# Kernel tuning notes

Hardware: AMD Instinct MI355X
Metric: run time of the kernel (lower is better)

The kernel has to match this reference:

```python
import jax, jax.numpy as jnp
import numpy as np

N_NODES = 100000
N_EDGES = 1600000
F_IN, F_HID, F_OUT = 64, 64, 32


def setup_inputs() -> dict:
    key = jax.random.key(0)
    k1, k2, k3, k4 = jax.random.split(key, 4)
    x = jax.random.normal(k1, (N_NODES, F_IN), dtype=jnp.float32)
    edge_idx = jax.random.randint(k2, (2, N_EDGES), 0, N_NODES, dtype=jnp.int64)
    W1 = jax.random.normal(k3, (F_IN, F_HID), dtype=jnp.float32) * (1.0 / np.sqrt(F_IN))
    b1 = jnp.zeros((F_HID,), dtype=jnp.float32)
    W2 = jax.random.normal(k4, (F_HID, F_OUT), dtype=jnp.float32) * (1.0 / np.sqrt(F_HID))
    b2 = jnp.zeros((F_OUT,), dtype=jnp.float32)
    return {"x": x, "edge_idx": edge_idx, "W1": W1, "b1": b1, "W2": W2, "b2": b2}


def _gcn_conv(h, src, dst, norm, W, b, n):
    # PyG GCNConv: transform first, then normalized sum aggregation, then bias.
    h = h @ W                                   # [N, F_out]
    msg = h[src] * norm[:, None]                # [E+N, F_out] gather + scale
    agg = jax.ops.segment_sum(msg, dst, num_segments=n)  # scatter-add
    return agg + b


def reference(x, edge_idx, W1, b1, W2, b2):
    n = x.shape[0]
    loop = jnp.arange(n, dtype=edge_idx.dtype)
    src = jnp.concatenate([edge_idx[0], loop])  # add self-loops
    dst = jnp.concatenate([edge_idx[1], loop])
    # symmetric normalization D^-1/2 (A+I) D^-1/2
    deg = jax.ops.segment_sum(jnp.ones_like(dst, dtype=x.dtype), dst, num_segments=n)
    dinv = jnp.where(deg > 0, jax.lax.rsqrt(deg), 0.0)
    norm = dinv[src] * dinv[dst]                # [E+N]

    h = _gcn_conv(x, src, dst, norm, W1, b1, n)
    h = jax.nn.relu(h)
    # dropout(p=0.5) is identity in eval mode (deterministic reference)
    out = _gcn_conv(h, src, dst, norm, W2, b2, n)
    return out
```

## Files before the change

### kernel.cpp

```cpp
#include <hip/hip_runtime.h>
#include <hip/hip_bf16.h>
#include <hip/hip_fp16.h>


#define N_FEAT_IN 64
#define B2SHIFT 9
#define CHUNK 4096
#define PADSTRIDE 3592

struct alignas(8) half4 { __half2 lo, hi; };
struct alignas(16) half8 { __half2 h[4]; };

__global__ __launch_bounds__(1024) void passA_hist(const int* __restrict__ dst,
                                                   int* __restrict__ H, int E) {
    __shared__ int h[256];
    int t = threadIdx.x;
    if (t < 256) h[t] = 0;
    __syncthreads();
    int base = blockIdx.x * CHUNK;
    int end = min(base + CHUNK, E);
    for (int i = base + t; i < end; i += 1024)
        atomicAdd(&h[dst[i] >> B2SHIFT], 1);
    __syncthreads();
    if (t < 256) H[blockIdx.x * 256 + t] = h[t];
}

__global__ __launch_bounds__(512) void col_scan_a(int* __restrict__ H,
                                                  int* __restrict__ ctot, int NR) {
    __shared__ int s[512];
    int b = blockIdx.x;
    int t = threadIdx.x;
    int v = (t < NR) ? H[t * 256 + b] : 0;
    s[t] = v;
    __syncthreads();
    for (int off = 1; off < 512; off <<= 1) {
        int a = (t >= off) ? s[t - off] : 0;
        __syncthreads();
        s[t] += a;
        __syncthreads();
    }
    if (t < NR) H[t * 256 + b] = s[t] - v;
    if (t == 511) ctot[b] = s[511];
}

__global__ __launch_bounds__(256) void col_scan_b(const int* __restrict__ ctot,
                                                  int* __restrict__ cbase,
                                                  int* __restrict__ bbase,
                                                  int* __restrict__ row_ptr,
                                                  int NB, int n, int E) {
    __shared__ int s[256];
    int t = threadIdx.x;
    int v = ctot[t];
    s[t] = v;
    __syncthreads();
    for (int off = 1; off < 256; off <<= 1) {
        int a = (t >= off) ? s[t - off] : 0;
        __syncthreads();
        s[t] += a;
        __syncthreads();
    }
    int e = s[t] - v;
    cbase[t] = e;
    if (t < NB) bbase[t] = e;
    if (t == 0) { bbase[NB] = E; row_ptr[n] = E; }
}

__global__ __launch_bounds__(1024) void passB_place(const int* __restrict__ src,
                                                    const int* __restrict__ dst,
                                                    const int* __restrict__ H,
                                                    const int* __restrict__ cbase,
                                                    unsigned* __restrict__ bedges, int E) {
    __shared__ int cur[256];
    int t = threadIdx.x;
    if (t < 256) cur[t] = H[blockIdx.x * 256 + t] + cbase[t];
    __syncthreads();
    int base = blockIdx.x * CHUNK;
    int end = min(base + CHUNK, E);
    for (int i = base + t; i < end; i += 1024) {
        int d = dst[i];
        int p = atomicAdd(&cur[d >> B2SHIFT], 1);
        bedges[p] = ((unsigned)src[i] << B2SHIFT) | (unsigned)(d & 511);
    }
}

__global__ __launch_bounds__(1024) void bucket_csr(const int* __restrict__ bbase,
                                                   const unsigned* __restrict__ bedges,
                                                   int* __restrict__ row_ptr,
                                                   int* __restrict__ rend,
                                                   float* __restrict__ dinv,
                                                   int* __restrict__ csr_src, int n) {
    __shared__ int lh[512];
    __shared__ int cur[512];
    int t = threadIdx.x;
    if (t < 512) lh[t] = 0;
    __syncthreads();
    int b = blockIdx.x;
    int beg = bbase[b], end = bbase[b + 1];
    for (int i = beg + t; i < end; i += 1024)
        atomicAdd(&lh[bedges[i] & 511], 1);
    __syncthreads();
    int c = (t < 512) ? lh[t] : 0;
    __syncthreads();
    int cp = (c + 7) & ~7;
    if (t < 512) lh[t] = cp;
    __syncthreads();
    for (int off = 1; off < 512; off <<= 1) {
        int a = (t < 512 && t >= off) ? lh[t - off] : 0;
        __syncthreads();
        if (t < 512) lh[t] += a;
        __syncthreads();
    }
    int pb = ((beg + 7) & ~7) + b * PADSTRIDE;
    if (t < 512) {
        int d = (b << B2SHIFT) + t;
        int rbeg = pb + lh[t] - cp;
        cur[t] = rbeg;
        if (d < n) {
            row_ptr[d] = rbeg;
            rend[d] = rbeg + cp;
            dinv[d] = rsqrtf((float)c + 1.0f);
            for (int i = c; i < cp; ++i) csr_src[rbeg + i] = n;
        }
    }
    __syncthreads();
    for (int i = beg + t; i < end; i += 1024) {
        unsigned v = bedges[i];
        int p = atomicAdd(&cur[v & 511], 1);
        csr_src[p] = (int)(v >> B2SHIFT);
    }
}

__global__ __launch_bounds__(256) void gemm64(const float* __restrict__ A,
                                              const float* __restrict__ W,
                                              const float* __restrict__ dinv,
                                              __half* __restrict__ outh, int n) {
    constexpr int K = 64, FO = 64, CPT = 16;
    __shared__ float As[64][K + 4];
    __shared__ float Ws[K][FO];

    const int t = threadIdx.x;
    const int r0 = blockIdx.x * 64;

    if (blockIdx.x == 0 && t < FO)
        outh[(size_t)n * FO + t] = __float2half(0.f);

    for (int i = t; i < K * FO / 4; i += 256) {
        int k = i / (FO / 4);
        int c4 = (i % (FO / 4)) * 4;
        *(float4*)&Ws[k][c4] = *(const float4*)&W[k * FO + c4];
    }
    for (int i = t; i < 1024; i += 256) {
        int row = i / 16;
        int c4 = (i % 16) * 4;
        int g = r0 + row;
        float4 v = make_float4(0.f, 0.f, 0.f, 0.f);
        if (g < n) v = *(const float4*)&A[(size_t)g * K + c4];
        *(float4*)&As[row][c4] = v;
    }
    __syncthreads();

    const int row = t >> 2;
    const int c0 = (t & 3) * CPT;
    float acc[CPT];
#pragma unroll
    for (int j = 0; j < CPT; ++j) acc[j] = 0.f;
#pragma unroll
    for (int k = 0; k < K; ++k) {
        float xv = As[row][k];
#pragma unroll
        for (int j = 0; j < CPT; ++j) acc[j] = fmaf(xv, Ws[k][c0 + j], acc[j]);
    }

    int g = r0 + row;
    if (g < n) {
        float sc = dinv[g];
#pragma unroll
        for (int j4 = 0; j4 < CPT; j4 += 4) {
            half4 h;
            h.lo = __floats2half2_rn(acc[j4] * sc, acc[j4 + 1] * sc);
            h.hi = __floats2half2_rn(acc[j4 + 2] * sc, acc[j4 + 3] * sc);
            *(half4*)&outh[(size_t)g * FO + c0 + j4] = h;
        }
    }
}

#define ACC8(v)                                                       \
    {                                                                 \
        float2 f0 = __half22float2((v).h[0]);                         \
        float2 f1 = __half22float2((v).h[1]);                         \
        float2 f2 = __half22float2((v).h[2]);                         \
        float2 f3 = __half22float2((v).h[3]);                         \
        a0 += f0.x; a1 += f0.y; a2 += f1.x; a3 += f1.y;               \
        a4 += f2.x; a5 += f2.y; a6 += f3.x; a7 += f3.y;               \
    }

__global__ __launch_bounds__(256) void agg64(const int* __restrict__ row_ptr,
                                             const int* __restrict__ rend,
                                             const int* __restrict__ csr_src,
                                             const float* __restrict__ dinv,
                                             const __half* __restrict__ xs1,
                                             const float* __restrict__ b1,
                                             __half* __restrict__ th, int n) {
    int d = blockIdx.x * 32 + (threadIdx.x >> 3);
    if (d >= n) return;
    int c = threadIdx.x & 7;
    const half8* __restrict__ xrow = (const half8*)xs1 + c;

    half8 sv = xrow[(size_t)d * 8];
    float a0, a1, a2, a3, a4, a5, a6, a7;
    {
        float2 f0 = __half22float2(sv.h[0]), f1 = __half22float2(sv.h[1]);
        float2 f2 = __half22float2(sv.h[2]), f3 = __half22float2(sv.h[3]);
        a0 = f0.x; a1 = f0.y; a2 = f1.x; a3 = f1.y;
        a4 = f2.x; a5 = f2.y; a6 = f3.x; a7 = f3.y;
    }

    int beg = row_ptr[d];
    int end = rend[d];
    if (beg < end) {
        int4 ia = *(const int4*)&csr_src[beg];
        int4 ib = *(const int4*)&csr_src[beg + 4];
        int jb = beg;
        for (;;) {
            int jn = jb + 8;
            bool more = jn < end;
            int js = more ? jn : beg;
            int4 na = *(const int4*)&csr_src[js];
            int4 nb = *(const int4*)&csr_src[js + 4];
            half8 v0 = xrow[(size_t)ia.x * 8];
            half8 v1 = xrow[(size_t)ia.y * 8];
            half8 v2 = xrow[(size_t)ia.z * 8];
            half8 v3 = xrow[(size_t)ia.w * 8];
            half8 v4 = xrow[(size_t)ib.x * 8];
            half8 v5 = xrow[(size_t)ib.y * 8];
            half8 v6 = xrow[(size_t)ib.z * 8];
            half8 v7 = xrow[(size_t)ib.w * 8];
            ACC8(v0); ACC8(v1); ACC8(v2); ACC8(v3);
            ACC8(v4); ACC8(v5); ACC8(v6); ACC8(v7);
            if (!more) break;
            jb = jn; ia = na; ib = nb;
        }
    }

    float di = dinv[d];
    float4 ba = *(const float4*)&b1[8 * c];
    float4 bb = *(const float4*)&b1[8 * c + 4];
    float t0 = fmaxf(fmaf(di, a0, ba.x), 0.f);
    float t1 = fmaxf(fmaf(di, a1, ba.y), 0.f);
    float t2 = fmaxf(fmaf(di, a2, ba.z), 0.f);
    float t3 = fmaxf(fmaf(di, a3, ba.w), 0.f);
    float t4 = fmaxf(fmaf(di, a4, bb.x), 0.f);
    float t5 = fmaxf(fmaf(di, a5, bb.y), 0.f);
    float t6 = fmaxf(fmaf(di, a6, bb.z), 0.f);
    float t7 = fmaxf(fmaf(di, a7, bb.w), 0.f);
    half8 o;
    o.h[0] = __floats2half2_rn(t0, t1);
    o.h[1] = __floats2half2_rn(t2, t3);
    o.h[2] = __floats2half2_rn(t4, t5);
    o.h[3] = __floats2half2_rn(t6, t7);
    *(half8*)&th[(size_t)d * 64 + 8 * c] = o;
}

__global__ __launch_bounds__(256) void gemm32h(const __half* __restrict__ Ah,
                                               const float* __restrict__ W,
                                               const float* __restrict__ dinv,
                                               __half* __restrict__ outh, int n) {
    constexpr int K = 64, FO = 32, CPT = 8;
    __shared__ float As[64][K + 4];
    __shared__ float Ws[K][FO];

    const int t = threadIdx.x;
    const int r0 = blockIdx.x * 64;

    if (blockIdx.x == 0 && t < FO)
        outh[(size_t)n * FO + t] = __float2half(0.f);

    for (int i = t; i < K * FO / 4; i += 256) {
        int k = i / (FO / 4);
        int c4 = (i % (FO / 4)) * 4;
        *(float4*)&Ws[k][c4] = *(const float4*)&W[k * FO + c4];
    }
    for (int i = t; i < 1024; i += 256) {
        int row = i / 16;
        int c4 = (i % 16) * 4;
        int g = r0 + row;
        float4 v = make_float4(0.f, 0.f, 0.f, 0.f);
        if (g < n) {
            half4 hv = *(const half4*)&Ah[(size_t)g * K + c4];
            float2 lo = __half22float2(hv.lo), hi = __half22float2(hv.hi);
            v = make_float4(lo.x, lo.y, hi.x, hi.y);
        }
        *(float4*)&As[row][c4] = v;
    }
    __syncthreads();

    const int row = t >> 2;
    const int c0 = (t & 3) * CPT;
    float acc[CPT];
#pragma unroll
    for (int j = 0; j < CPT; ++j) acc[j] = 0.f;
#pragma unroll
    for (int k = 0; k < K; ++k) {
        float xv = As[row][k];
#pragma unroll
        for (int j = 0; j < CPT; ++j) acc[j] = fmaf(xv, Ws[k][c0 + j], acc[j]);
    }

    int g = r0 + row;
    if (g < n) {
        float sc = dinv[g];
#pragma unroll
        for (int j4 = 0; j4 < CPT; j4 += 4) {
            half4 h;
            h.lo = __floats2half2_rn(acc[j4] * sc, acc[j4 + 1] * sc);
            h.hi = __floats2half2_rn(acc[j4 + 2] * sc, acc[j4 + 3] * sc);
            *(half4*)&outh[(size_t)g * FO + c0 + j4] = h;
        }
    }
}

__global__ __launch_bounds__(256) void agg32(const int* __restrict__ row_ptr,
                                             const int* __restrict__ rend,
                                             const int* __restrict__ csr_src,
                                             const float* __restrict__ dinv,
                                             const __half* __restrict__ xs2,
                                             const float* __restrict__ b2,
                                             float* __restrict__ out, int n) {
    int d = blockIdx.x * 64 + (threadIdx.x >> 2);
    if (d >= n) return;
    int c = threadIdx.x & 3;
    const half8* __restrict__ xrow = (const half8*)xs2 + c;

    half8 sv = xrow[(size_t)d * 4];
    float a0, a1, a2, a3, a4, a5, a6, a7;
    {
        float2 f0 = __half22float2(sv.h[0]), f1 = __half22float2(sv.h[1]);
        float2 f2 = __half22float2(sv.h[2]), f3 = __half22float2(sv.h[3]);
        a0 = f0.x; a1 = f0.y; a2 = f1.x; a3 = f1.y;
        a4 = f2.x; a5 = f2.y; a6 = f3.x; a7 = f3.y;
    }

    int beg = row_ptr[d];
    int end = rend[d];
    if (beg < end) {
        int4 ia = *(const int4*)&csr_src[beg];
        int4 ib = *(const int4*)&csr_src[beg + 4];
        int jb = beg;
        for (;;) {
            int jn = jb + 8;
            bool more = jn < end;
            int js = more ? jn : beg;
            int4 na = *(const int4*)&csr_src[js];
            int4 nb = *(const int4*)&csr_src[js + 4];
            half8 v0 = xrow[(size_t)ia.x * 4];
            half8 v1 = xrow[(size_t)ia.y * 4];
            half8 v2 = xrow[(size_t)ia.z * 4];
            half8 v3 = xrow[(size_t)ia.w * 4];
            half8 v4 = xrow[(size_t)ib.x * 4];
            half8 v5 = xrow[(size_t)ib.y * 4];
            half8 v6 = xrow[(size_t)ib.z * 4];
            half8 v7 = xrow[(size_t)ib.w * 4];
            ACC8(v0); ACC8(v1); ACC8(v2); ACC8(v3);
            ACC8(v4); ACC8(v5); ACC8(v6); ACC8(v7);
            if (!more) break;
            jb = jn; ia = na; ib = nb;
        }
    }

    float di = dinv[d];
    float4 ba = *(const float4*)&b2[8 * c];
    float4 bb = *(const float4*)&b2[8 * c + 4];
    float4 r0, r1;
    r0.x = fmaf(di, a0, ba.x);
    r0.y = fmaf(di, a1, ba.y);
    r0.z = fmaf(di, a2, ba.z);
    r0.w = fmaf(di, a3, ba.w);
    r1.x = fmaf(di, a4, bb.x);
    r1.y = fmaf(di, a5, bb.y);
    r1.z = fmaf(di, a6, bb.z);
    r1.w = fmaf(di, a7, bb.w);
    *(float4*)&out[(size_t)d * 32 + 8 * c] = r0;
    *(float4*)&out[(size_t)d * 32 + 8 * c + 4] = r1;
}

extern "C" void kernel_launch(void* const* d_in, const int* in_sizes, int n_in,
                              void* d_out, int out_size, void* d_ws, size_t ws_size,
                              hipStream_t stream) {
    const float* x  = (const float*)d_in[0];
    const int*   ei = (const int*)d_in[1];
    const float* W1 = (const float*)d_in[2];
    const float* b1 = (const float*)d_in[3];
    const float* W2 = (const float*)d_in[4];
    const float* b2 = (const float*)d_in[5];
    float* out = (float*)d_out;

    const int n = in_sizes[0] / N_FEAT_IN;
    const int E = in_sizes[1] / 2;
    const int* srcI = ei;
    const int* dstI = ei + E;

    const int NB = (n + 511) >> B2SHIFT;
    const int NR = (E + CHUNK - 1) / CHUNK;

    char* ws = (char*)d_ws;
    size_t off = 0;
    auto alloc = [&](size_t bytes) {
        void* p = ws + off;
        off += (bytes + 255) & ~(size_t)255;
        return p;
    };
    float*    dinv    = (float*)alloc((size_t)n * 4);
    int*      row_ptr = (int*)alloc((size_t)(n + 1) * 4);
    int*      rend    = (int*)alloc((size_t)n * 4);
    int*      bbase   = (int*)alloc((size_t)(NB + 1) * 4);
    int*      ctot    = (int*)alloc((size_t)256 * 4);
    int*      cbase   = (int*)alloc((size_t)256 * 4);
    int*      H       = (int*)alloc((size_t)NR * 256 * 4);
    unsigned* bedges  = (unsigned*)alloc((size_t)E * 4);
    int*      csr_src = (int*)alloc((size_t)(E + (size_t)NB * PADSTRIDE + 16) * 4);
    __half*   xs1     = (__half*)alloc((size_t)(n + 1) * 64 * 2);
    __half*   th      = (__half*)alloc((size_t)n * 64 * 2);
    __half*   xs2     = (__half*)alloc((size_t)(n + 1) * 32 * 2);

    passA_hist<<<NR, 1024, 0, stream>>>(dstI, H, E);
    col_scan_a<<<256, 512, 0, stream>>>(H, ctot, NR);
    col_scan_b<<<1, 256, 0, stream>>>(ctot, cbase, bbase, row_ptr, NB, n, E);
    passB_place<<<NR, 1024, 0, stream>>>(srcI, dstI, H, cbase, bedges, E);

    bucket_csr<<<NB, 1024, 0, stream>>>(bbase, bedges, row_ptr, rend, dinv, csr_src, n);

    gemm64<<<(n + 63) / 64, 256, 0, stream>>>(x, W1, dinv, xs1, n);

    agg64<<<(n + 31) / 32, 256, 0, stream>>>(row_ptr, rend, csr_src, dinv, xs1, b1, th, n);

    gemm32h<<<(n + 63) / 64, 256, 0, stream>>>(th, W2, dinv, xs2, n);

    agg32<<<(n + 63) / 64, 256, 0, stream>>>(row_ptr, rend, csr_src, dinv, xs2, b2, out, n);
}
```

Before: 204.9 us.

## Fuse CSR build into one cooperative kernel with LDS-staged bucket writes

Replaces the five CSR-construction launches (histogram, two scans, placement, bucket CSR) with a single cooperative kernel of 256 blocks that uses grid.sync between phases. The per-bucket scatter now goes into an LDS staging buffer and is then written to global memory in order, falling back to direct global scatter when a bucket overflows the buffer. The two dense GEMM inner loops are also changed to read A and W from shared memory as float4. This removes launch gaps and random global writes, at the cost of grid-wide barriers, fewer blocks (less parallelism for the histogram and placement phases) and large LDS use that may limit occupancy.

```diff
diff --git a/kernel.cpp b/kernel.cpp
--- a/kernel.cpp
+++ b/kernel.cpp
@@ -1,107 +1,99 @@
 #include <hip/hip_runtime.h>
+#include <hip/hip_cooperative_groups.h>
 #include <hip/hip_bf16.h>
 #include <hip/hip_fp16.h>
 
+namespace cg = cooperative_groups;
+
 
 #define N_FEAT_IN 64
 #define B2SHIFT 9
-#define CHUNK 4096
+#define NBLK 256
 #define PADSTRIDE 3592
+#define STCAP 12288
 
 struct alignas(8) half4 { __half2 lo, hi; };
 struct alignas(16) half8 { __half2 h[4]; };
 
-__global__ __launch_bounds__(1024) void passA_hist(const int* __restrict__ dst,
-                                                   int* __restrict__ H, int E) {
-    __shared__ int h[256];
-    int t = threadIdx.x;
-    if (t < 256) h[t] = 0;
-    __syncthreads();
-    int base = blockIdx.x * CHUNK;
-    int end = min(base + CHUNK, E);
-    for (int i = base + t; i < end; i += 1024)
-        atomicAdd(&h[dst[i] >> B2SHIFT], 1);
-    __syncthreads();
-    if (t < 256) H[blockIdx.x * 256 + t] = h[t];
-}
-
-__global__ __launch_bounds__(512) void col_scan_a(int* __restrict__ H,
-                                                  int* __restrict__ ctot, int NR) {
-    __shared__ int s[512];
-    int b = blockIdx.x;
-    int t = threadIdx.x;
-    int v = (t < NR) ? H[t * 256 + b] : 0;
-    s[t] = v;
-    __syncthreads();
-    for (int off = 1; off < 512; off <<= 1) {
-        int a = (t >= off) ? s[t - off] : 0;
-        __syncthreads();
-        s[t] += a;
-        __syncthreads();
-    }
-    if (t < NR) H[t * 256 + b] = s[t] - v;
-    if (t == 511) ctot[b] = s[511];
-}
-
-__global__ __launch_bounds__(256) void col_scan_b(const int* __restrict__ ctot,
-                                                  int* __restrict__ cbase,
-                                                  int* __restrict__ bbase,
-                                                  int* __restrict__ row_ptr,
-                                                  int NB, int n, int E) {
-    __shared__ int s[256];
-    int t = threadIdx.x;
-    int v = ctot[t];
-    s[t] = v;
-    __syncthreads();
-    for (int off = 1; off < 256; off <<= 1) {
-        int a = (t >= off) ? s[t - off] : 0;
-        __syncthreads();
-        s[t] += a;
-        __syncthreads();
-    }
-    int e = s[t] - v;
-    cbase[t] = e;
-    if (t < NB) bbase[t] = e;
-    if (t == 0) { bbase[NB] = E; row_ptr[n] = E; }
-}
-
-__global__ __launch_bounds__(1024) void passB_place(const int* __restrict__ src,
-                                                    const int* __restrict__ dst,
-                                                    const int* __restrict__ H,
-                                                    const int* __restrict__ cbase,
-                                                    unsigned* __restrict__ bedges, int E) {
-    __shared__ int cur[256];
-    int t = threadIdx.x;
-    if (t < 256) cur[t] = H[blockIdx.x * 256 + t] + cbase[t];
-    __syncthreads();
-    int base = blockIdx.x * CHUNK;
-    int end = min(base + CHUNK, E);
-    for (int i = base + t; i < end; i += 1024) {
+__global__ __launch_bounds__(1024) void build_coop(
+    const int* __restrict__ src, const int* __restrict__ dst,
+    int* __restrict__ H, int* __restrict__ ctot, int* __restrict__ cbase,
+    int* __restrict__ bbase, unsigned* __restrict__ bedges,
+    int* __restrict__ row_ptr, int* __restrict__ rend,
+    float* __restrict__ dinv, int* __restrict__ csr_src,
+    int n, int E, int NB)
+{
+    cg::grid_group grid = cg::this_grid();
+    __shared__ int smem[1024 + STCAP];
+    const int t = threadIdx.x;
+    const int b = blockIdx.x;
+    const int EC = (E + NBLK - 1) / NBLK;
+    const int base = b * EC, endE = min(base + EC, E);
+
+    if (t < 256) smem[t] = 0;
+    __syncthreads();
+    for (int i = base + t; i < endE; i += 1024)
+        atomicAdd(&smem[dst[i] >> B2SHIFT], 1);
+    __syncthreads();
+    if (t < 256) H[b * 256 + t] = smem[t];
+    grid.sync();
+
+    {
+        int v = 0;
+        if (t < 256) { v = H[t * 256 + b]; smem[t] = v; }
+        __syncthreads();
+        for (int off = 1; off < 256; off <<= 1) {
+            int a = (t < 256 && t >= off) ? smem[t - off] : 0;
+            __syncthreads();
+            if (t < 256) smem[t] += a;
+            __syncthreads();
+        }
+        if (t < 256) H[t * 256 + b] = smem[t] - v;
+        if (t == 255) ctot[b] = smem[255];
+    }
+    grid.sync();
+
+    if (b == 0) {
+        int v = 0;
+        if (t < 256) { v = ctot[t]; smem[t] = v; }
+        __syncthreads();
+        for (int off = 1; off < 256; off <<= 1) {
+            int a = (t < 256 && t >= off) ? smem[t - off] : 0;
+            __syncthreads();
+            if (t < 256) smem[t] += a;
+            __syncthreads();
+        }
+        if (t < 256) {
+            int e = smem[t] - v;
+            cbase[t] = e;
+            if (t < NB) bbase[t] = e;
+        }
+        if (t == 0) { bbase[NB] = E; row_ptr[n] = E; }
+    }
+    grid.sync();
+
+    if (t < 256) smem[t] = H[b * 256 + t] + cbase[t];
+    __syncthreads();
+    for (int i = base + t; i < endE; i += 1024) {
         int d = dst[i];
-        int p = atomicAdd(&cur[d >> B2SHIFT], 1);
+        int p = atomicAdd(&smem[d >> B2SHIFT], 1);
         bedges[p] = ((unsigned)src[i] << B2SHIFT) | (unsigned)(d & 511);
     }
-}
-
-__global__ __launch_bounds__(1024) void bucket_csr(const int* __restrict__ bbase,
-                                                   const unsigned* __restrict__ bedges,
-                                                   int* __restrict__ row_ptr,
-                                                   int* __restrict__ rend,
-                                                   float* __restrict__ dinv,
-                                                   int* __restrict__ csr_src, int n) {
-    __shared__ int lh[512];
-    __shared__ int cur[512];
-    int t = threadIdx.x;
+    grid.sync();
+
+    if (b >= NB) return;
+    int* lh    = smem;
+    int* cur   = smem + 512;
+    int* stage = smem + 1024;
     if (t < 512) lh[t] = 0;
     __syncthreads();
-    int b = blockIdx.x;
-    int beg = bbase[b], end = bbase[b + 1];
+    const int beg = bbase[b], end = bbase[b + 1];
     for (int i = beg + t; i < end; i += 1024)
         atomicAdd(&lh[bedges[i] & 511], 1);
     __syncthreads();
-    int c = (t < 512) ? lh[t] : 0;
-    __syncthreads();
-    int cp = (c + 7) & ~7;
+    const int c = (t < 512) ? lh[t] : 0;
+    __syncthreads();
+    const int cp = (c + 7) & ~7;
     if (t < 512) lh[t] = cp;
     __syncthreads();
     for (int off = 1; off < 512; off <<= 1) {
@@ -110,23 +102,44 @@
         if (t < 512) lh[t] += a;
         __syncthreads();
     }
-    int pb = ((beg + 7) & ~7) + b * PADSTRIDE;
+    const int padTotal = lh[511];
+    const int pb = ((beg + 7) & ~7) + b * PADSTRIDE;
+    int rbeg = 0;
     if (t < 512) {
         int d = (b << B2SHIFT) + t;
-        int rbeg = pb + lh[t] - cp;
-        cur[t] = rbeg;
+        rbeg = pb + lh[t] - cp;
         if (d < n) {
             row_ptr[d] = rbeg;
             rend[d] = rbeg + cp;
             dinv[d] = rsqrtf((float)c + 1.0f);
-            for (int i = c; i < cp; ++i) csr_src[rbeg + i] = n;
-        }
-    }
-    __syncthreads();
-    for (int i = beg + t; i < end; i += 1024) {
-        unsigned v = bedges[i];
-        int p = atomicAdd(&cur[v & 511], 1);
-        csr_src[p] = (int)(v >> B2SHIFT);
+        }
+    }
+    __syncthreads();
+    if (padTotal <= STCAP) {
+        if (t < 512) cur[t] = rbeg - pb;
+        for (int i = t; i < padTotal; i += 1024) stage[i] = n;
+        __syncthreads();
+        for (int i = beg + t; i < end; i += 1024) {
+            unsigned v = bedges[i];
+            int p = atomicAdd(&cur[v & 511], 1);
+            stage[p] = (int)(v >> B2SHIFT);
+        }
+        __syncthreads();
+        for (int i = t; i < padTotal; i += 1024)
+            csr_src[pb + i] = stage[i];
+    } else {
+        if (t < 512) {
+            cur[t] = rbeg;
+            int d = (b << B2SHIFT) + t;
+            if (d < n)
+                for (int i = c; i < cp; ++i) csr_src[rbeg + i] = n;
+        }
+        __syncthreads();
+        for (int i = beg + t; i < end; i += 1024) {
+            unsigned v = bedges[i];
+            int p = atomicAdd(&cur[v & 511], 1);
+            csr_src[p] = (int)(v >> B2SHIFT);
+        }
     }
 }
 
@@ -165,10 +178,32 @@
 #pragma unroll
     for (int j = 0; j < CPT; ++j) acc[j] = 0.f;
 #pragma unroll
-    for (int k = 0; k < K; ++k) {
-        float xv = As[row][k];
-#pragma unroll
-        for (int j = 0; j < CPT; ++j) acc[j] = fmaf(xv, Ws[k][c0 + j], acc[j]);
+    for (int k4 = 0; k4 < K; k4 += 4) {
+        float4 xv4 = *(const float4*)&As[row][k4];
+#pragma unroll
+        for (int kk = 0; kk < 4; ++kk) {
+            float xv = (kk == 0) ? xv4.x : (kk == 1) ? xv4.y : (kk == 2) ? xv4.z : xv4.w;
+            float4 w0 = *(const float4*)&Ws[k4 + kk][c0];
+            float4 w1 = *(const float4*)&Ws[k4 + kk][c0 + 4];
+            float4 w2 = *(const float4*)&Ws[k4 + kk][c0 + 8];
+            float4 w3 = *(const float4*)&Ws[k4 + kk][c0 + 12];
+            acc[0]  = fmaf(xv, w0.x, acc[0]);
+            acc[1]  = fmaf(xv, w0.y, acc[1]);
+            acc[2]  = fmaf(xv, w0.z, acc[2]);
+            acc[3]  = fmaf(xv, w0.w, acc[3]);
+            acc[4]  = fmaf(xv, w1.x, acc[4]);
+            acc[5]  = fmaf(xv, w1.y, acc[5]);
+            acc[6]  = fmaf(xv, w1.z, acc[6]);
+            acc[7]  = fmaf(xv, w1.w, acc[7]);
+            acc[8]  = fmaf(xv, w2.x, acc[8]);
+            acc[9]  = fmaf(xv, w2.y, acc[9]);
+            acc[10] = fmaf(xv, w2.z, acc[10]);
+            acc[11] = fmaf(xv, w2.w, acc[11]);
+            acc[12] = fmaf(xv, w3.x, acc[12]);
+            acc[13] = fmaf(xv, w3.y, acc[13]);
+            acc[14] = fmaf(xv, w3.z, acc[14]);
+            acc[15] = fmaf(xv, w3.w, acc[15]);
+        }
     }
 
     int g = r0 + row;
@@ -300,10 +335,22 @@
 #pragma unroll
     for (int j = 0; j < CPT; ++j) acc[j] = 0.f;
 #pragma unroll
-    for (int k = 0; k < K; ++k) {
-        float xv = As[row][k];
-#pragma unroll
-        for (int j = 0; j < CPT; ++j) acc[j] = fmaf(xv, Ws[k][c0 + j], acc[j]);
+    for (int k4 = 0; k4 < K; k4 += 4) {
+        float4 xv4 = *(const float4*)&As[row][k4];
+#pragma unroll
+        for (int kk = 0; kk < 4; ++kk) {
+            float xv = (kk == 0) ? xv4.x : (kk == 1) ? xv4.y : (kk == 2) ? xv4.z : xv4.w;
+            float4 w0 = *(const float4*)&Ws[k4 + kk][c0];
+            float4 w1 = *(const float4*)&Ws[k4 + kk][c0 + 4];
+            acc[0] = fmaf(xv, w0.x, acc[0]);
+            acc[1] = fmaf(xv, w0.y, acc[1]);
+            acc[2] = fmaf(xv, w0.z, acc[2]);
+            acc[3] = fmaf(xv, w0.w, acc[3]);
+            acc[4] = fmaf(xv, w1.x, acc[4]);
+            acc[5] = fmaf(xv, w1.y, acc[5]);
+            acc[6] = fmaf(xv, w1.z, acc[6]);
+            acc[7] = fmaf(xv, w1.w, acc[7]);
+        }
     }
 
     int g = r0 + row;
@@ -400,7 +447,6 @@
     const int* dstI = ei + E;
 
     const int NB = (n + 511) >> B2SHIFT;
-    const int NR = (E + CHUNK - 1) / CHUNK;
 
     char* ws = (char*)d_ws;
     size_t off = 0;
@@ -415,19 +461,22 @@
     int*      bbase   = (int*)alloc((size_t)(NB + 1) * 4);
     int*      ctot    = (int*)alloc((size_t)256 * 4);
     int*      cbase   = (int*)alloc((size_t)256 * 4);
-    int*      H       = (int*)alloc((size_t)NR * 256 * 4);
+    int*      H       = (int*)alloc((size_t)NBLK * 256 * 4);
     unsigned* bedges  = (unsigned*)alloc((size_t)E * 4);
     int*      csr_src = (int*)alloc((size_t)(E + (size_t)NB * PADSTRIDE + 16) * 4);
     __half*   xs1     = (__half*)alloc((size_t)(n + 1) * 64 * 2);
     __half*   th      = (__half*)alloc((size_t)n * 64 * 2);
     __half*   xs2     = (__half*)alloc((size_t)(n + 1) * 32 * 2);
 
-    passA_hist<<<NR, 1024, 0, stream>>>(dstI, H, E);
-    col_scan_a<<<256, 512, 0, stream>>>(H, ctot, NR);
-    col_scan_b<<<1, 256, 0, stream>>>(ctot, cbase, bbase, row_ptr, NB, n, E);
-    passB_place<<<NR, 1024, 0, stream>>>(srcI, dstI, H, cbase, bedges, E);
-
-    bucket_csr<<<NB, 1024, 0, stream>>>(bbase, bedges, row_ptr, rend, dinv, csr_src, n);
+    {
+        int n_ = n, E_ = E, NB_ = NB;
+        void* args[] = {
+            (void*)&srcI, (void*)&dstI, (void*)&H, (void*)&ctot, (void*)&cbase,
+            (void*)&bbase, (void*)&bedges, (void*)&row_ptr, (void*)&rend,
+            (void*)&dinv, (void*)&csr_src, (void*)&n_, (void*)&E_, (void*)&NB_};
+        hipLaunchCooperativeKernel((const void*)build_coop, dim3(NBLK), dim3(1024),
+                                   args, 0, stream);
+    }
 
     gemm64<<<(n + 63) / 64, 256, 0, stream>>>(x, W1, dinv, xs1, n);
 
```

After: 319.5 us. 1.56x slower.

## Split feature tables into 16-column slabs and aggregate each slab separately

Applied to the files above, without the earlier changes.

Stores the fp16 transformed features in column slabs of 16 features per node (32 bytes per row) and runs the aggregation kernels once per slab. Each pass gathers from a smaller table (about 3.2 MB per slab), which should fit better in L2 and the infinity cache. The cost is re-reading the CSR index lists four or two times and running more kernel launches. The GEMM inner loops are also changed to use float4 LDS reads.

```diff
diff --git a/kernel.cpp b/kernel.cpp
--- a/kernel.cpp
+++ b/kernel.cpp
@@ -9,7 +9,6 @@
 #define PADSTRIDE 3592
 
 struct alignas(8) half4 { __half2 lo, hi; };
-struct alignas(16) half8 { __half2 h[4]; };
 
 __global__ __launch_bounds__(1024) void passA_hist(const int* __restrict__ dst,
                                                    int* __restrict__ H, int E) {
@@ -133,16 +132,17 @@
 __global__ __launch_bounds__(256) void gemm64(const float* __restrict__ A,
                                               const float* __restrict__ W,
                                               const float* __restrict__ dinv,
-                                              __half* __restrict__ outh, int n) {
+                                              __half* __restrict__ xs1, int n) {
     constexpr int K = 64, FO = 64, CPT = 16;
     __shared__ float As[64][K + 4];
     __shared__ float Ws[K][FO];
 
     const int t = threadIdx.x;
     const int r0 = blockIdx.x * 64;
+    const size_t slabE = (size_t)(n + 1) * 16;
 
     if (blockIdx.x == 0 && t < FO)
-        outh[(size_t)n * FO + t] = __float2half(0.f);
+        xs1[(size_t)(t >> 4) * slabE + (size_t)n * 16 + (t & 15)] = __float2half(0.f);
 
     for (int i = t; i < K * FO / 4; i += 256) {
         int k = i / (FO / 4);
@@ -165,10 +165,32 @@
 #pragma unroll
     for (int j = 0; j < CPT; ++j) acc[j] = 0.f;
 #pragma unroll
-    for (int k = 0; k < K; ++k) {
-        float xv = As[row][k];
-#pragma unroll
-        for (int j = 0; j < CPT; ++j) acc[j] = fmaf(xv, Ws[k][c0 + j], acc[j]);
+    for (int k4 = 0; k4 < K; k4 += 4) {
+        float4 xv4 = *(const float4*)&As[row][k4];
+#pragma unroll
+        for (int kk = 0; kk < 4; ++kk) {
+            float xv = (kk == 0) ? xv4.x : (kk == 1) ? xv4.y : (kk == 2) ? xv4.z : xv4.w;
+            float4 w0 = *(const float4*)&Ws[k4 + kk][c0];
+            float4 w1 = *(const float4*)&Ws[k4 + kk][c0 + 4];
+            float4 w2 = *(const float4*)&Ws[k4 + kk][c0 + 8];
+            float4 w3 = *(const float4*)&Ws[k4 + kk][c0 + 12];
+            acc[0]  = fmaf(xv, w0.x, acc[0]);
+            acc[1]  = fmaf(xv, w0.y, acc[1]);
+            acc[2]  = fmaf(xv, w0.z, acc[2]);
+            acc[3]  = fmaf(xv, w0.w, acc[3]);
+            acc[4]  = fmaf(xv, w1.x, acc[4]);
+            acc[5]  = fmaf(xv, w1.y, acc[5]);
+            acc[6]  = fmaf(xv, w1.z, acc[6]);
+            acc[7]  = fmaf(xv, w1.w, acc[7]);
+            acc[8]  = fmaf(xv, w2.x, acc[8]);
+            acc[9]  = fmaf(xv, w2.y, acc[9]);
+            acc[10] = fmaf(xv, w2.z, acc[10]);
+            acc[11] = fmaf(xv, w2.w, acc[11]);
+            acc[12] = fmaf(xv, w3.x, acc[12]);
+            acc[13] = fmaf(xv, w3.y, acc[13]);
+            acc[14] = fmaf(xv, w3.z, acc[14]);
+            acc[15] = fmaf(xv, w3.w, acc[15]);
+        }
     }
 
     int g = r0 + row;
@@ -176,43 +198,39 @@
         float sc = dinv[g];
 #pragma unroll
         for (int j4 = 0; j4 < CPT; j4 += 4) {
+            int cc = c0 + j4;
             half4 h;
             h.lo = __floats2half2_rn(acc[j4] * sc, acc[j4 + 1] * sc);
             h.hi = __floats2half2_rn(acc[j4 + 2] * sc, acc[j4 + 3] * sc);
-            *(half4*)&outh[(size_t)g * FO + c0 + j4] = h;
-        }
-    }
-}
-
-#define ACC8(v)                                                       \
+            *(half4*)&xs1[(size_t)(cc >> 4) * slabE + (size_t)g * 16 + (cc & 15)] = h;
+        }
+    }
+}
+
+#define ACC4(v)                                                       \
     {                                                                 \
-        float2 f0 = __half22float2((v).h[0]);                         \
-        float2 f1 = __half22float2((v).h[1]);                         \
-        float2 f2 = __half22float2((v).h[2]);                         \
-        float2 f3 = __half22float2((v).h[3]);                         \
+        float2 f0 = __half22float2((v).lo);                           \
+        float2 f1 = __half22float2((v).hi);                           \
         a0 += f0.x; a1 += f0.y; a2 += f1.x; a3 += f1.y;               \
-        a4 += f2.x; a5 += f2.y; a6 += f3.x; a7 += f3.y;               \
-    }
-
-__global__ __launch_bounds__(256) void agg64(const int* __restrict__ row_ptr,
-                                             const int* __restrict__ rend,
-                                             const int* __restrict__ csr_src,
-                                             const float* __restrict__ dinv,
-                                             const __half* __restrict__ xs1,
-                                             const float* __restrict__ b1,
-                                             __half* __restrict__ th, int n) {
-    int d = blockIdx.x * 32 + (threadIdx.x >> 3);
+    }
+
+__global__ __launch_bounds__(256) void agg64s(const int* __restrict__ row_ptr,
+                                              const int* __restrict__ rend,
+                                              const int* __restrict__ csr_src,
+                                              const float* __restrict__ dinv,
+                                              const __half* __restrict__ xslab,
+                                              const float* __restrict__ b1f,
+                                              __half* __restrict__ tslab, int n) {
+    int d = blockIdx.x * 64 + (threadIdx.x >> 2);
     if (d >= n) return;
-    int c = threadIdx.x & 7;
-    const half8* __restrict__ xrow = (const half8*)xs1 + c;
-
-    half8 sv = xrow[(size_t)d * 8];
-    float a0, a1, a2, a3, a4, a5, a6, a7;
+    int c = threadIdx.x & 3;
+    const half4* __restrict__ xrow = (const half4*)xslab + c;
+
+    half4 sv = xrow[(size_t)d * 4];
+    float a0, a1, a2, a3;
     {
-        float2 f0 = __half22float2(sv.h[0]), f1 = __half22float2(sv.h[1]);
-        float2 f2 = __half22float2(sv.h[2]), f3 = __half22float2(sv.h[3]);
+        float2 f0 = __half22float2(sv.lo), f1 = __half22float2(sv.hi);
         a0 = f0.x; a1 = f0.y; a2 = f1.x; a3 = f1.y;
-        a4 = f2.x; a5 = f2.y; a6 = f3.x; a7 = f3.y;
     }
 
     int beg = row_ptr[d];
@@ -227,53 +245,48 @@
             int js = more ? jn : beg;
             int4 na = *(const int4*)&csr_src[js];
             int4 nb = *(const int4*)&csr_src[js + 4];
-            half8 v0 = xrow[(size_t)ia.x * 8];
-            half8 v1 = xrow[(size_t)ia.y * 8];
-            half8 v2 = xrow[(size_t)ia.z * 8];
-            half8 v3 = xrow[(size_t)ia.w * 8];
-            half8 v4 = xrow[(size_t)ib.x * 8];
-            half8 v5 = xrow[(size_t)ib.y * 8];
-            half8 v6 = xrow[(size_t)ib.z * 8];
-            half8 v7 = xrow[(size_t)ib.w * 8];
-            ACC8(v0); ACC8(v1); ACC8(v2); ACC8(v3);
-            ACC8(v4); ACC8(v5); ACC8(v6); ACC8(v7);
+            half4 v0 = xrow[(size_t)ia.x * 4];
+            half4 v1 = xrow[(size_t)ia.y * 4];
+            half4 v2 = xrow[(size_t)ia.z * 4];
+            half4 v3 = xrow[(size_t)ia.w * 4];
+            half4 v4 = xrow[(size_t)ib.x * 4];
+            half4 v5 = xrow[(size_t)ib.y * 4];
+            half4 v6 = xrow[(size_t)ib.z * 4];
+            half4 v7 = xrow[(size_t)ib.w * 4];
+            ACC4(v0); ACC4(v1); ACC4(v2); ACC4(v3);
+            ACC4(v4); ACC4(v5); ACC4(v6); ACC4(v7);
             if (!more) break;
             jb = jn; ia = na; ib = nb;
         }
     }
 
     float di = dinv[d];
-    float4 ba = *(const float4*)&b1[8 * c];
-    float4 bb = *(const float4*)&b1[8 * c + 4];
-    float t0 = fmaxf(fmaf(di, a0, ba.x), 0.f);
-    float t1 = fmaxf(fmaf(di, a1, ba.y), 0.f);
-    float t2 = fmaxf(fmaf(di, a2, ba.z), 0.f);
-    float t3 = fmaxf(fmaf(di, a3, ba.w), 0.f);
-    float t4 = fmaxf(fmaf(di, a4, bb.x), 0.f);
-    float t5 = fmaxf(fmaf(di, a5, bb.y), 0.f);
-    float t6 = fmaxf(fmaf(di, a6, bb.z), 0.f);
-    float t7 = fmaxf(fmaf(di, a7, bb.w), 0.f);
-    half8 o;
-    o.h[0] = __floats2half2_rn(t0, t1);
-    o.h[1] = __floats2half2_rn(t2, t3);
-    o.h[2] = __floats2half2_rn(t4, t5);
-    o.h[3] = __floats2half2_rn(t6, t7);
-    *(half8*)&th[(size_t)d * 64 + 8 * c] = o;
-}
-
-__global__ __launch_bounds__(256) void gemm32h(const __half* __restrict__ Ah,
+    float4 bv = *(const float4*)&b1f[4 * c];
+    float t0 = fmaxf(fmaf(di, a0, bv.x), 0.f);
+    float t1 = fmaxf(fmaf(di, a1, bv.y), 0.f);
+    float t2 = fmaxf(fmaf(di, a2, bv.z), 0.f);
+    float t3 = fmaxf(fmaf(di, a3, bv.w), 0.f);
+    half4 o;
+    o.lo = __floats2half2_rn(t0, t1);
+    o.hi = __floats2half2_rn(t2, t3);
+    *(half4*)&tslab[(size_t)d * 16 + 4 * c] = o;
+}
+
+__global__ __launch_bounds__(256) void gemm32h(const __half* __restrict__ th,
                                                const float* __restrict__ W,
                                                const float* __restrict__ dinv,
-                                               __half* __restrict__ outh, int n) {
+                                               __half* __restrict__ xs2, int n) {
     constexpr int K = 64, FO = 32, CPT = 8;
     __shared__ float As[64][K + 4];
     __shared__ float Ws[K][FO];
 
     const int t = threadIdx.x;
     const int r0 = blockIdx.x * 64;
+    const size_t slabE = (size_t)(n + 1) * 16;
+    const size_t tslabE = (size_t)n * 16;
 
     if (blockIdx.x == 0 && t < FO)
-        outh[(size_t)n * FO + t] = __float2half(0.f);
+        xs2[(size_t)(t >> 4) * slabE + (size_t)n * 16 + (t & 15)] = __float2half(0.f);
 
     for (int i = t; i < K * FO / 4; i += 256) {
         int k = i / (FO / 4);
@@ -286,7 +299,8 @@
         int g = r0 + row;
         float4 v = make_float4(0.f, 0.f, 0.f, 0.f);
         if (g < n) {
-            half4 hv = *(const half4*)&Ah[(size_t)g * K + c4];
+            const __half* thp = th + (size_t)(c4 >> 4) * tslabE;
+            half4 hv = *(const half4*)&thp[(size_t)g * 16 + (c4 & 15)];
             float2 lo = __half22float2(hv.lo), hi = __half22float2(hv.hi);
             v = make_float4(lo.x, lo.y, hi.x, hi.y);
         }
@@ -300,10 +314,22 @@
 #pragma unroll
     for (int j = 0; j < CPT; ++j) acc[j] = 0.f;
 #pragma unroll
-    for (int k = 0; k < K; ++k) {
-        float xv = As[row][k];
-#pragma unroll
-        for (int j = 0; j < CPT; ++j) acc[j] = fmaf(xv, Ws[k][c0 + j], acc[j]);
+    for (int k4 = 0; k4 < K; k4 += 4) {
+        float4 xv4 = *(const float4*)&As[row][k4];
+#pragma unroll
+        for (int kk = 0; kk < 4; ++kk) {
+            float xv = (kk == 0) ? xv4.x : (kk == 1) ? xv4.y : (kk == 2) ? xv4.z : xv4.w;
+            float4 w0 = *(const float4*)&Ws[k4 + kk][c0];
+            float4 w1 = *(const float4*)&Ws[k4 + kk][c0 + 4];
+            acc[0] = fmaf(xv, w0.x, acc[0]);
+            acc[1] = fmaf(xv, w0.y, acc[1]);
+            acc[2] = fmaf(xv, w0.z, acc[2]);
+            acc[3] = fmaf(xv, w0.w, acc[3]);
+            acc[4] = fmaf(xv, w1.x, acc[4]);
+            acc[5] = fmaf(xv, w1.y, acc[5]);
+            acc[6] = fmaf(xv, w1.z, acc[6]);
+            acc[7] = fmaf(xv, w1.w, acc[7]);
+        }
     }
 
     int g = r0 + row;
@@ -311,33 +337,32 @@
         float sc = dinv[g];
 #pragma unroll
         for (int j4 = 0; j4 < CPT; j4 += 4) {
+            int cc = c0 + j4;
             half4 h;
             h.lo = __floats2half2_rn(acc[j4] * sc, acc[j4 + 1] * sc);
             h.hi = __floats2half2_rn(acc[j4 + 2] * sc, acc[j4 + 3] * sc);
-            *(half4*)&outh[(size_t)g * FO + c0 + j4] = h;
-        }
-    }
-}
-
-__global__ __launch_bounds__(256) void agg32(const int* __restrict__ row_ptr,
-                                             const int* __restrict__ rend,
-                                             const int* __restrict__ csr_src,
-                                             const float* __restrict__ dinv,
-                                             const __half* __restrict__ xs2,
-                                             const float* __restrict__ b2,
-                                             float* __restrict__ out, int n) {
+            *(half4*)&xs2[(size_t)(cc >> 4) * slabE + (size_t)g * 16 + (cc & 15)] = h;
+        }
+    }
+}
+
+__global__ __launch_bounds__(256) void agg32s(const int* __restrict__ row_ptr,
+                                              const int* __restrict__ rend,
+                                              const int* __restrict__ csr_src,
+                                              const float* __restrict__ dinv,
+                                              const __half* __restrict__ xslab,
+                                              const float* __restrict__ b2s,
+                                              float* __restrict__ outp, int n) {
     int d = blockIdx.x * 64 + (threadIdx.x >> 2);
     if (d >= n) return;
     int c = threadIdx.x & 3;
-    const half8* __restrict__ xrow = (const half8*)xs2 + c;
-
-    half8 sv = xrow[(size_t)d * 4];
-    float a0, a1, a2, a3, a4, a5, a6, a7;
+    const half4* __restrict__ xrow = (const half4*)xslab + c;
+
+    half4 sv = xrow[(size_t)d * 4];
+    float a0, a1, a2, a3;
     {
-        float2 f0 = __half22float2(sv.h[0]), f1 = __half22float2(sv.h[1]);
-        float2 f2 = __half22float2(sv.h[2]), f3 = __half22float2(sv.h[3]);
+        float2 f0 = __half22float2(sv.lo), f1 = __half22float2(sv.hi);
         a0 = f0.x; a1 = f0.y; a2 = f1.x; a3 = f1.y;
-        a4 = f2.x; a5 = f2.y; a6 = f3.x; a7 = f3.y;
     }
 
     int beg = row_ptr[d];
@@ -352,35 +377,29 @@
             int js = more ? jn : beg;
             int4 na = *(const int4*)&csr_src[js];
             int4 nb = *(const int4*)&csr_src[js + 4];
-            half8 v0 = xrow[(size_t)ia.x * 4];
-            half8 v1 = xrow[(size_t)ia.y * 4];
-            half8 v2 = xrow[(size_t)ia.z * 4];
-            half8 v3 = xrow[(size_t)ia.w * 4];
-            half8 v4 = xrow[(size_t)ib.x * 4];
-            half8 v5 = xrow[(size_t)ib.y * 4];
-            half8 v6 = xrow[(size_t)ib.z * 4];
-            half8 v7 = xrow[(size_t)ib.w * 4];
-            ACC8(v0); ACC8(v1); ACC8(v2); ACC8(v3);
-            ACC8(v4); ACC8(v5); ACC8(v6); ACC8(v7);
+            half4 v0 = xrow[(size_t)ia.x * 4];
+            half4 v1 = xrow[(size_t)ia.y * 4];
+            half4 v2 = xrow[(size_t)ia.z * 4];
+            half4 v3 = xrow[(size_t)ia.w * 4];
+            half4 v4 = xrow[(size_t)ib.x * 4];
+            half4 v5 = xrow[(size_t)ib.y * 4];
+            half4 v6 = xrow[(size_t)ib.z * 4];
+            half4 v7 = xrow[(size_t)ib.w * 4];
+            ACC4(v0); ACC4(v1); ACC4(v2); ACC4(v3);
+            ACC4(v4); ACC4(v5); ACC4(v6); ACC4(v7);
             if (!more) break;
             jb = jn; ia = na; ib = nb;
         }
     }
 
     float di = dinv[d];
-    float4 ba = *(const float4*)&b2[8 * c];
-    float4 bb = *(const float4*)&b2[8 * c + 4];
-    float4 r0, r1;
-    r0.x = fmaf(di, a0, ba.x);
-    r0.y = fmaf(di, a1, ba.y);
-    r0.z = fmaf(di, a2, ba.z);
-    r0.w = fmaf(di, a3, ba.w);
-    r1.x = fmaf(di, a4, bb.x);
-    r1.y = fmaf(di, a5, bb.y);
-    r1.z = fmaf(di, a6, bb.z);
-    r1.w = fmaf(di, a7, bb.w);
-    *(float4*)&out[(size_t)d * 32 + 8 * c] = r0;
-    *(float4*)&out[(size_t)d * 32 + 8 * c + 4] = r1;
+    float4 bv = *(const float4*)&b2s[4 * c];
+    float4 r;
+    r.x = fmaf(di, a0, bv.x);
+    r.y = fmaf(di, a1, bv.y);
+    r.z = fmaf(di, a2, bv.z);
+    r.w = fmaf(di, a3, bv.w);
+    *(float4*)&outp[(size_t)d * 32 + 4 * c] = r;
 }
 
 extern "C" void kernel_launch(void* const* d_in, const int* in_sizes, int n_in,
@@ -422,6 +441,9 @@
     __half*   th      = (__half*)alloc((size_t)n * 64 * 2);
     __half*   xs2     = (__half*)alloc((size_t)(n + 1) * 32 * 2);
 
+    const size_t slab1 = (size_t)(n + 1) * 16;
+    const size_t slabT = (size_t)n * 16;
+
     passA_hist<<<NR, 1024, 0, stream>>>(dstI, H, E);
     col_scan_a<<<256, 512, 0, stream>>>(H, ctot, NR);
     col_scan_b<<<1, 256, 0, stream>>>(ctot, cbase, bbase, row_ptr, NB, n, E);
@@ -431,9 +453,17 @@
 
     gemm64<<<(n + 63) / 64, 256, 0, stream>>>(x, W1, dinv, xs1, n);
 
-    agg64<<<(n + 31) / 32, 256, 0, stream>>>(row_ptr, rend, csr_src, dinv, xs1, b1, th, n);
+    for (int f = 0; f < 4; ++f)
+        agg64s<<<(n + 63) / 64, 256, 0, stream>>>(row_ptr, rend, csr_src, dinv,
+                                                  xs1 + (size_t)f * slab1,
+                                                  b1 + 16 * f,
+                                                  th + (size_t)f * slabT, n);
 
     gemm32h<<<(n + 63) / 64, 256, 0, stream>>>(th, W2, dinv, xs2, n);
 
-    agg32<<<(n + 63) / 64, 256, 0, stream>>>(row_ptr, rend, csr_src, dinv, xs2, b2, out, n);
-}
+    for (int s = 0; s < 2; ++s)
+        agg32s<<<(n + 63) / 64, 256, 0, stream>>>(row_ptr, rend, csr_src, dinv,
+                                                  xs2 + (size_t)s * slab1,
+                                                  b2 + 16 * s,
+                                                  out + 16 * s, n);
+}
```

Measured after the change: 245.4 us. 1.2x slower.
